# Kernel tuning notes

Measured on AMD Instinct MI355X. Metric: run time of the kernel, lower is better.

The kernel has to match this reference:

```python
import jax, jax.numpy as jnp
import numpy as np

INPUT_DIM = 128
DEPTH = 6
HIDDEN = 64
NUM_INNER = 2 ** DEPTH - 1  # 63
NUM_LEAVES = 2 ** DEPTH     # 64


def setup_inputs() -> dict:
    key = jax.random.key(0)
    ks = jax.random.split(key, 6)
    x = jax.random.normal(ks[0], (65536, INPUT_DIM), dtype=jnp.float32)
    s1 = 1.0 / np.sqrt(INPUT_DIM)
    s2 = 1.0 / np.sqrt(HIDDEN)
    W1 = jax.random.uniform(ks[1], (NUM_INNER, INPUT_DIM, HIDDEN), minval=-s1, maxval=s1, dtype=jnp.float32)
    b1 = jax.random.uniform(ks[2], (NUM_INNER, HIDDEN), minval=-s1, maxval=s1, dtype=jnp.float32)
    W2 = jax.random.uniform(ks[3], (NUM_INNER, HIDDEN), minval=-s2, maxval=s2, dtype=jnp.float32)
    b2 = jax.random.uniform(ks[4], (NUM_INNER,), minval=-s2, maxval=s2, dtype=jnp.float32)
    leaf = jax.random.normal(ks[5], (NUM_LEAVES, 1), dtype=jnp.float32)
    return {"x": x, "W1": W1, "b1": b1, "W2": W2, "b2": b2, "leaf": leaf}


def reference(x, W1, b1, W2, b2, leaf):
    # All inner-node MLPs as one batched GEMM pair: [B, N] node probabilities
    h = jax.nn.relu(jnp.einsum('bi,nih->bnh', x, W1) + b1)      # [B, N, H]
    probs = jax.nn.sigmoid(jnp.einsum('bnh,nh->bn', h, W2) + b2)  # [B, N]

    # Original code walks node_idx = 2*node_idx+1 unconditionally, so the chain
    # of used node indices is 2^k - 1 for k = 0..depth-1.
    chain = jnp.array([2 ** k - 1 for k in range(DEPTH)], dtype=jnp.int32)
    p_chain = probs[:, chain]  # [B, D]

    # Bit k (LSB first) of leaf index selects p (bit=1) vs 1-p (bit=0)
    leaves = np.arange(NUM_LEAVES)
    bits = jnp.asarray(((leaves[:, None] >> np.arange(DEPTH)[None, :]) & 1).astype(np.float32))  # [L, D]

    # path_probs[b, l] = prod_k ( bits[l,k]*p + (1-bits[l,k])*(1-p) )
    factors = bits[None, :, :] * p_chain[:, None, :] + (1.0 - bits[None, :, :]) * (1.0 - p_chain[:, None, :])  # [B, L, D]
    path_probs = jnp.prod(factors, axis=-1)  # [B, L]

    return (path_probs @ leaf)[:, 0]  # [B]
```

## Files before the change

kernel.cpp:

```cpp
#include <hip/hip_runtime.h>

typedef __attribute__((ext_vector_type(4))) float f32x4;
typedef __attribute__((ext_vector_type(8))) short bf16x8;
typedef __attribute__((ext_vector_type(4))) unsigned int u32x4;

#define IDIM    128
#define HID     64
#define TDEPTH  6
#define WROWS   32
#define NWAVES  4
#define BLOCK   (NWAVES * 64)
#define MROWS   (WROWS * NWAVES)
#define NODE_ELEMS 8192
#define WFRAG_ELEMS (TDEPTH * NODE_ELEMS)

__device__ __forceinline__ unsigned short f2bf(float f) {
    unsigned int u = __builtin_bit_cast(unsigned int, f);
    unsigned int r = (u + 0x7FFFu + ((u >> 16) & 1u)) >> 16;
    return (unsigned short)r;
}

__device__ __forceinline__ unsigned int f2bf_pk(float f0, float f1) {
    unsigned int u0 = __builtin_bit_cast(unsigned int, f0);
    unsigned int u1 = __builtin_bit_cast(unsigned int, f1);
    unsigned int t0 = u0 + 0x7FFFu + ((u0 >> 16) & 1u);
    unsigned int t1 = u1 + 0x7FFFu + ((u1 >> 16) & 1u);
    return (t1 & 0xFFFF0000u) | (t0 >> 16);
}

__global__ void prep_wfrag(const float* __restrict__ W1, unsigned short* __restrict__ wfrag) {
    int idx = blockIdx.x * 256 + threadIdx.x;
    if (idx >= WFRAG_ELEMS) return;
    int j    = idx & 7;
    int lane = (idx >> 3) & 63;
    int ct   = (idx >> 9) & 3;
    int ks   = (idx >> 11) & 3;
    int nd   = idx >> 13;
    int node = (1 << nd) - 1;
    int k    = ks * 32 + (lane >> 4) * 8 + j;
    int col  = ct * 16 + (lane & 15);
    wfrag[idx] = f2bf(W1[(node * IDIM + k) * HID + col]);
}

template <bool USE_WS>
__global__ __launch_bounds__(BLOCK, 3)
void sdt_kernel(const float* __restrict__ x, const float* __restrict__ W1,
                const float* __restrict__ b1, const float* __restrict__ W2,
                const float* __restrict__ b2, const float* __restrict__ leaf,
                const unsigned short* __restrict__ wfrag, float* __restrict__ out) {
    __shared__ __align__(16) unsigned short bs[2][NODE_ELEMS];
    __shared__ float p_lds[NWAVES][WROWS][8];
    __shared__ float leaf_lds[64];

    const int tid  = threadIdx.x;
    const int wave = tid >> 6;
    const int lane = tid & 63;
    const int lcol = lane & 15;
    const int lq   = lane >> 4;
    const int m0   = blockIdx.x * MROWS + wave * WROWS;

    const float* xb = x + (size_t)(m0 + lcol) * IDIM + lq * 8;
    float4 araw[2][4][2];
    #pragma unroll
    for (int rt = 0; rt < 2; rt++)
        #pragma unroll
        for (int ks = 0; ks < 4; ks++) {
            const float4* ap = reinterpret_cast<const float4*>(
                xb + (size_t)(rt * 16) * IDIM + ks * 32);
            araw[rt][ks][0] = ap[0];
            araw[rt][ks][1] = ap[1];
        }

    auto stage = [&](int buf, int nd) {
        if (USE_WS) {
            const u32x4* src = reinterpret_cast<const u32x4*>(wfrag + nd * NODE_ELEMS);
            u32x4* dst = reinterpret_cast<u32x4*>(&bs[buf][0]);
            #pragma unroll
            for (int i = 0; i < (NODE_ELEMS * 2 / 16) / BLOCK; i++)
                dst[tid + i * BLOCK] = src[tid + i * BLOCK];
        } else {
            int node = (1 << nd) - 1;
            for (int e = tid; e < NODE_ELEMS; e += BLOCK) {
                int j = e & 7, ln = (e >> 3) & 63, ct = (e >> 9) & 3, ks = e >> 11;
                int k   = ks * 32 + (ln >> 4) * 8 + j;
                int col = ct * 16 + (ln & 15);
                bs[buf][e] = f2bf(W1[((size_t)node * IDIM + k) * HID + col]);
            }
        }
    };
    stage(0, 0);
    if (tid < 64) leaf_lds[tid] = leaf[tid];

    bf16x8 afrag[2][4];
    #pragma unroll
    for (int rt = 0; rt < 2; rt++)
        #pragma unroll
        for (int ks = 0; ks < 4; ks++) {
            float4 v0 = araw[rt][ks][0], v1 = araw[rt][ks][1];
            u32x4 pk;
            pk[0] = f2bf_pk(v0.x, v0.y);
            pk[1] = f2bf_pk(v0.z, v0.w);
            pk[2] = f2bf_pk(v1.x, v1.y);
            pk[3] = f2bf_pk(v1.z, v1.w);
            afrag[rt][ks] = __builtin_bit_cast(bf16x8, pk);
        }

    __syncthreads();

    #pragma unroll
    for (int nd = 0; nd < TDEPTH; nd++) {
        const int buf = nd & 1;
        if (nd + 1 < TDEPTH) stage(buf ^ 1, nd + 1);

        const int node = (1 << nd) - 1;
        float b1v[4], w2v[4];
        #pragma unroll
        for (int ct = 0; ct < 4; ct++) {
            int col = ct * 16 + lcol;
            b1v[ct] = b1[node * HID + col];
            w2v[ct] = W2[node * HID + col];
        }
        const float bias2 = b2[node];

        f32x4 acc[2][4];
        #pragma unroll
        for (int rt = 0; rt < 2; rt++)
            #pragma unroll
            for (int ct = 0; ct < 4; ct++)
                acc[rt][ct] = (f32x4){0.f, 0.f, 0.f, 0.f};
        #pragma unroll
        for (int ks = 0; ks < 4; ks++) {
            bf16x8 bfrag[4];
            #pragma unroll
            for (int ct = 0; ct < 4; ct++)
                bfrag[ct] = *reinterpret_cast<const bf16x8*>(
                    &bs[buf][(ks * 4 + ct) * 512 + lane * 8]);
            #pragma unroll
            for (int rt = 0; rt < 2; rt++)
                #pragma unroll
                for (int ct = 0; ct < 4; ct++)
                    acc[rt][ct] = __builtin_amdgcn_mfma_f32_16x16x32_bf16(
                        afrag[rt][ks], bfrag[ct], acc[rt][ct], 0, 0, 0);
        }

        #pragma unroll
        for (int rt = 0; rt < 2; rt++) {
            #pragma unroll
            for (int r = 0; r < 4; r++) {
                float s = 0.f;
                #pragma unroll
                for (int ct = 0; ct < 4; ct++) {
                    float v = acc[rt][ct][r] + b1v[ct];
                    v = v > 0.f ? v : 0.f;
                    s += v * w2v[ct];
                }
                #pragma unroll
                for (int d = 1; d < 16; d <<= 1)
                    s += __shfl_xor(s, d, 64);
                float p = 1.f / (1.f + __expf(-(s + bias2)));
                if (lcol == 0)
                    p_lds[wave][rt * 16 + lq * 4 + r][nd] = p;
            }
        }
        __syncthreads();
    }

    if (tid < MROWS) {
        const int wv = tid >> 5, row = tid & 31;
        float q0 = p_lds[wv][row][0];
        float q1 = p_lds[wv][row][1];
        float q2 = p_lds[wv][row][2];
        float q3 = p_lds[wv][row][3];
        float p4 = p_lds[wv][row][4];
        float p5 = p_lds[wv][row][5];
        float acc_out = 0.f;
        #pragma unroll
        for (int ch = 0; ch < 4; ch++) {
            float f4 = (ch & 1) ? p4 : 1.f - p4;
            float f5 = (ch & 2) ? p5 : 1.f - p5;
            const float* lf = leaf_lds + ch * 16;
            float tt[8];
            #pragma unroll
            for (int j = 0; j < 8; j++) {
                float a = lf[2 * j], b = lf[2 * j + 1];
                tt[j] = a + q0 * (b - a);
            }
            #pragma unroll
            for (int j = 0; j < 4; j++) tt[j] = tt[2 * j] + q1 * (tt[2 * j + 1] - tt[2 * j]);
            #pragma unroll
            for (int j = 0; j < 2; j++) tt[j] = tt[2 * j] + q2 * (tt[2 * j + 1] - tt[2 * j]);
            float s = tt[0] + q3 * (tt[1] - tt[0]);
            acc_out += f4 * f5 * s;
        }
        out[(size_t)blockIdx.x * MROWS + tid] = acc_out;
    }
}

extern "C" void kernel_launch(void* const* d_in, const int* in_sizes, int n_in,
                              void* d_out, int out_size, void* d_ws, size_t ws_size,
                              hipStream_t stream) {
    const float* x    = (const float*)d_in[0];
    const float* W1   = (const float*)d_in[1];
    const float* b1   = (const float*)d_in[2];
    const float* W2   = (const float*)d_in[3];
    const float* b2   = (const float*)d_in[4];
    const float* leaf = (const float*)d_in[5];
    float* out = (float*)d_out;

    const int Bn = in_sizes[0] / IDIM;
    const int nblocks = Bn / MROWS;

    if (ws_size >= (size_t)WFRAG_ELEMS * sizeof(unsigned short)) {
        unsigned short* wfrag = (unsigned short*)d_ws;
        prep_wfrag<<<(WFRAG_ELEMS + 255) / 256, 256, 0, stream>>>(W1, wfrag);
        sdt_kernel<true><<<nblocks, BLOCK, 0, stream>>>(x, W1, b1, W2, b2, leaf, wfrag, out);
    } else {
        sdt_kernel<false><<<nblocks, BLOCK, 0, stream>>>(x, W1, b1, W2, b2, leaf, nullptr, out);
    }
}
```

Baseline: 99.39 us.

## Use 8-wave blocks staging three node weights at once with fewer barriers

```diff
diff --git a/kernel.cpp b/kernel.cpp
--- a/kernel.cpp
+++ b/kernel.cpp
@@ -8,7 +8,7 @@
 #define HID     64
 #define TDEPTH  6
 #define WROWS   32
-#define NWAVES  4
+#define NWAVES  8
 #define BLOCK   (NWAVES * 64)
 #define MROWS   (WROWS * NWAVES)
 #define NODE_ELEMS 8192
@@ -43,13 +43,16 @@
 }
 
 template <bool USE_WS>
-__global__ __launch_bounds__(BLOCK, 3)
+__global__ __launch_bounds__(BLOCK, 2)
 void sdt_kernel(const float* __restrict__ x, const float* __restrict__ W1,
                 const float* __restrict__ b1, const float* __restrict__ W2,
                 const float* __restrict__ b2, const float* __restrict__ leaf,
                 const unsigned short* __restrict__ wfrag, float* __restrict__ out) {
-    __shared__ __align__(16) unsigned short bs[2][NODE_ELEMS];
-    __shared__ float p_lds[NWAVES][WROWS][8];
+    __shared__ __align__(16) unsigned short bs[3 * NODE_ELEMS];
+    __shared__ float p_lds[NWAVES][WROWS][9];
+    __shared__ float b1s[TDEPTH][HID];
+    __shared__ float w2s[TDEPTH][HID];
+    __shared__ float b2s[8];
     __shared__ float leaf_lds[64];
 
     const int tid  = threadIdx.x;
@@ -71,24 +74,33 @@
             araw[rt][ks][1] = ap[1];
         }
 
-    auto stage = [&](int buf, int nd) {
+    auto stage3 = [&](int nd0) {
         if (USE_WS) {
-            const u32x4* src = reinterpret_cast<const u32x4*>(wfrag + nd * NODE_ELEMS);
-            u32x4* dst = reinterpret_cast<u32x4*>(&bs[buf][0]);
-            #pragma unroll
-            for (int i = 0; i < (NODE_ELEMS * 2 / 16) / BLOCK; i++)
+            const u32x4* src = reinterpret_cast<const u32x4*>(
+                wfrag + (size_t)nd0 * NODE_ELEMS);
+            u32x4* dst = reinterpret_cast<u32x4*>(&bs[0]);
+            #pragma unroll
+            for (int i = 0; i < 6; i++)
                 dst[tid + i * BLOCK] = src[tid + i * BLOCK];
         } else {
-            int node = (1 << nd) - 1;
-            for (int e = tid; e < NODE_ELEMS; e += BLOCK) {
-                int j = e & 7, ln = (e >> 3) & 63, ct = (e >> 9) & 3, ks = e >> 11;
-                int k   = ks * 32 + (ln >> 4) * 8 + j;
-                int col = ct * 16 + (ln & 15);
-                bs[buf][e] = f2bf(W1[((size_t)node * IDIM + k) * HID + col]);
+            for (int e = tid; e < 3 * NODE_ELEMS; e += BLOCK) {
+                int j = e & 7, ln = (e >> 3) & 63, ct = (e >> 9) & 3,
+                    ks = (e >> 11) & 3, ndl = e >> 13;
+                int node = (1 << (nd0 + ndl)) - 1;
+                int k    = ks * 32 + (ln >> 4) * 8 + j;
+                int col  = ct * 16 + (ln & 15);
+                bs[e] = f2bf(W1[((size_t)node * IDIM + k) * HID + col]);
             }
         }
     };
-    stage(0, 0);
+
+    stage3(0);
+    if (tid < 384) {
+        int nd = tid >> 6, col = tid & 63, node = (1 << nd) - 1;
+        b1s[nd][col] = b1[node * HID + col];
+        w2s[nd][col] = W2[node * HID + col];
+    }
+    if (tid < 6)  b2s[tid] = b2[(1 << tid) - 1];
     if (tid < 64) leaf_lds[tid] = leaf[tid];
 
     bf16x8 afrag[2][4];
@@ -107,21 +119,7 @@
 
     __syncthreads();
 
-    #pragma unroll
-    for (int nd = 0; nd < TDEPTH; nd++) {
-        const int buf = nd & 1;
-        if (nd + 1 < TDEPTH) stage(buf ^ 1, nd + 1);
-
-        const int node = (1 << nd) - 1;
-        float b1v[4], w2v[4];
-        #pragma unroll
-        for (int ct = 0; ct < 4; ct++) {
-            int col = ct * 16 + lcol;
-            b1v[ct] = b1[node * HID + col];
-            w2v[ct] = W2[node * HID + col];
-        }
-        const float bias2 = b2[node];
-
+    auto compute = [&](int nd, int ndl) {
         f32x4 acc[2][4];
         #pragma unroll
         for (int rt = 0; rt < 2; rt++)
@@ -134,7 +132,7 @@
             #pragma unroll
             for (int ct = 0; ct < 4; ct++)
                 bfrag[ct] = *reinterpret_cast<const bf16x8*>(
-                    &bs[buf][(ks * 4 + ct) * 512 + lane * 8]);
+                    &bs[ndl * NODE_ELEMS + (ks * 4 + ct) * 512 + lane * 8]);
             #pragma unroll
             for (int rt = 0; rt < 2; rt++)
                 #pragma unroll
@@ -143,6 +141,13 @@
                         afrag[rt][ks], bfrag[ct], acc[rt][ct], 0, 0, 0);
         }
 
+        float b1v[4], w2v[4];
+        #pragma unroll
+        for (int ct = 0; ct < 4; ct++) {
+            b1v[ct] = b1s[nd][ct * 16 + lcol];
+            w2v[ct] = w2s[nd][ct * 16 + lcol];
+        }
+        const float bias2 = b2s[nd];
         #pragma unroll
         for (int rt = 0; rt < 2; rt++) {
             #pragma unroll
@@ -162,8 +167,16 @@
                     p_lds[wave][rt * 16 + lq * 4 + r][nd] = p;
             }
         }
-        __syncthreads();
-    }
+    };
+
+    #pragma unroll 1
+    for (int nd = 0; nd < 3; nd++) compute(nd, nd);
+    __syncthreads();
+    stage3(3);
+    __syncthreads();
+    #pragma unroll 1
+    for (int nd = 3; nd < 6; nd++) compute(nd, nd - 3);
+    __syncthreads();
 
     if (tid < MROWS) {
         const int wv = tid >> 5, row = tid & 31;
```

Result: no change. 101.3 us (+1.9%).
